# Kernel tuning notes

Hardware: AMD Instinct MI355X
Metric: run time of the kernel (lower is better)

## Reference

```python
import jax, jax.numpy as jnp
import numpy as np

NX, NY, T, TP, D, C = 1024, 1024, 512, 512, 128, 8


def _make_dtw_path(t_len, p_len, rng):
    """Random monotone warping path matrix from (0,0) to (t_len-1,p_len-1), as in init_DTW_matrix."""
    M = np.zeros((t_len, p_len), dtype=np.float32)
    k, l = 0, 0
    M[0, 0] = 1.0
    while (k < t_len - 1) or (l < p_len - 1):
        if k == t_len - 1:
            l += 1
        elif l == p_len - 1:
            k += 1
        else:
            m = rng.integers(3)
            if m == 0:
                k += 1
            elif m == 1:
                l += 1
            else:
                k += 1
                l += 1
        M[k, l] = 1.0
    return M


def setup_inputs() -> dict:
    key = jax.random.key(0)
    kx, ky, kc = jax.random.split(key, 3)
    X = jax.random.normal(kx, (NX, T, D), dtype=jnp.float32)
    Y = jax.random.normal(ky, (NY, TP, D), dtype=jnp.float32)
    classe = jax.random.randint(kc, (NX,), 0, C, dtype=jnp.int32)
    rng = np.random.default_rng(0)
    pi = jnp.asarray(np.stack([_make_dtw_path(T, TP, rng) for _ in range(C)]))  # [C, T, TP]
    return {"X": X, "Y": Y, "pi": pi, "classe": classe}


def reference(X, Y, pi, classe):
    """Fused OT-DTW l2 cost matrix: mat_cost[i,j] = sum_{t,tp,d} pi[cl(i)][t,tp]*(X[i,t,d]-Y[j,tp,d])^2.
    Equivalent to OTDTW.mat_cost_OT with metric='l2' (multi-dim branch), vectorized over classes."""
    pi_i = pi[classe]                              # [NX, T, TP] per-sample path matrix
    row = pi_i.sum(-1)                             # [NX, T]  row sums of path
    col = pi.sum(1)                                # [C, TP]  column sums per class
    C1 = jnp.einsum('itd,it->i', X * X, row)       # [NX]
    C2 = jnp.einsum('jpd,cp->cj', Y * Y, col)      # [C, NY]
    XP = jnp.einsum('itd,itp->ipd', X, pi_i)       # [NX, TP, D]
    C3 = jnp.einsum('ipd,jpd->ij', XP, Y)          # [NX, NY]
    return C1[:, None] + C2[classe] - 2.0 * C3
```

## Files before the change

kernel.cpp:

```cpp
#include <hip/hip_runtime.h>
#include <hip/hip_bf16.h>
#include <stdint.h>

namespace {

constexpr int kNX = 1024, kNY = 1024, kT = 512, kTP = 512, kD = 128, kC = 8;
constexpr int kK = kTP * kD;
constexpr int SPLITK = 16;
constexpr int KCH = kK / SPLITK;
constexpr int BKT = 64;
constexpr int NT = KCH / BKT;

typedef short bf16x8 __attribute__((ext_vector_type(8)));
typedef float f32x4 __attribute__((ext_vector_type(4)));

constexpr size_t OFF_YB  = 0;
constexpr size_t OFF_XP  = OFF_YB + (size_t)kNY * kK * 2;
constexpr size_t OFF_TS  = OFF_XP + (size_t)kNX * kK * 2;
constexpr size_t OFF_TE  = OFF_TS + (size_t)kC * kTP * 4;
constexpr size_t OFF_C1  = OFF_TE + (size_t)kC * kTP * 4;
constexpr size_t OFF_C2  = OFF_C1 + (size_t)kNX * 4;

__device__ __forceinline__ void gload16(const __hip_bfloat16* g, __hip_bfloat16* l) {
    __builtin_amdgcn_global_load_lds(
        (const __attribute__((address_space(1))) unsigned int*)g,
        (__attribute__((address_space(3))) unsigned int*)l, 16, 0, 0);
}

__device__ __forceinline__ unsigned short bf(float x) {
    union { __hip_bfloat16 h; unsigned short u; } cv;
    cv.h = __float2bfloat16(x);
    return cv.u;
}

__global__ void init_ranges(int* __restrict__ ts, int* __restrict__ te,
                            float* __restrict__ C1) {
    const int idx = blockIdx.x * 256 + threadIdx.x;
    if (idx < kC * kTP) { ts[idx] = 0x7fffffff; te[idx] = -1; }
    if (idx < kNX) C1[idx] = 0.f;
}

__global__ void pi_scan(const float* __restrict__ pi, int* __restrict__ ts,
                        int* __restrict__ te) {
    const int c = blockIdx.y;
    const int tbase = blockIdx.x * 64;
    const int p = threadIdx.x;
    const float* pic = pi + (size_t)c * kT * kTP;
    int tmin = 0x7fffffff, tmax = -1;
    for (int tt = 0; tt < 64; ++tt) {
        const int t = tbase + tt;
        float v = pic[(size_t)t * kTP + p];
        if (v != 0.f) { if (t < tmin) tmin = t; tmax = t; }
    }
    if (tmax >= 0) {
        atomicMin(&ts[c * kTP + p], tmin);
        atomicMax(&te[c * kTP + p], tmax);
    }
}

__global__ __launch_bounds__(256) void prep_main(const float* __restrict__ Y,
                                                 const float* __restrict__ X,
                                                 const int* __restrict__ classe,
                                                 const int* __restrict__ ts,
                                                 const int* __restrict__ te,
                                                 __hip_bfloat16* __restrict__ YB,
                                                 __hip_bfloat16* __restrict__ XPB,
                                                 float* __restrict__ C1,
                                                 float* __restrict__ C2) {
    const int bid = blockIdx.x;
    const int tid = threadIdx.x;
    const int sub = tid & 31, g = tid >> 5;

    if (bid < kNY) {
        const int j = bid;
        __shared__ float cntL[kC * kTP];
        for (int idx = tid; idx < kC * kTP; idx += 256)
            cntL[idx] = (float)(te[idx] - ts[idx] + 1);
        __syncthreads();

        const float4* Yj = (const float4*)(Y + (size_t)j * kTP * kD);
        unsigned short* YBj = (unsigned short*)YB + (size_t)j * kTP * kD;
        float c2acc[kC] = {};
        for (int p = g; p < kTP; p += 8) {
            float4 y = Yj[p * 32 + sub];
            ushort4 o;
            o.x = bf(y.x); o.y = bf(y.y); o.z = bf(y.z); o.w = bf(y.w);
            *(ushort4*)(YBj + p * kD + sub * 4) = o;
            float s = y.x * y.x + y.y * y.y + y.z * y.z + y.w * y.w;
            #pragma unroll
            for (int o2 = 16; o2; o2 >>= 1) s += __shfl_xor(s, o2, 32);
            if (sub == 0) {
                #pragma unroll
                for (int c = 0; c < kC; ++c) c2acc[c] += cntL[c * kTP + p] * s;
            }
        }
        __syncthreads();
        __shared__ float c2red[8][kC];
        if (sub == 0) {
            #pragma unroll
            for (int c = 0; c < kC; ++c) c2red[g][c] = c2acc[c];
        }
        __syncthreads();
        if (tid < kC) {
            float s = 0.f;
            #pragma unroll
            for (int q = 0; q < 8; ++q) s += c2red[q][tid];
            C2[tid * kNY + j] = s;
        }
    } else {
        const int b2 = bid - kNY;
        const int x8 = b2 & 7, r = b2 >> 3;
        const int pc = r & 7, i = (r >> 3) * 8 + x8;
        const int c = classe[i];
        const float4* Xi = (const float4*)(X + (size_t)i * kT * kD);
        unsigned short* XPi = (unsigned short*)XPB + (size_t)i * kTP * kD;
        int t0v[8], t1v[8];
        #pragma unroll
        for (int q = 0; q < 8; ++q) {
            const int p = pc * 64 + q * 8 + g;
            t0v[q] = ts[c * kTP + p];
            t1v[q] = te[c * kTP + p];
        }
        float sq = 0.f;
        #pragma unroll
        for (int q = 0; q < 8; ++q) {
            const int p = pc * 64 + q * 8 + g;
            float ax = 0.f, ay = 0.f, az = 0.f, aw = 0.f;
            for (int t = t0v[q]; t <= t1v[q]; ++t) {
                float4 v = Xi[t * 32 + sub];
                ax += v.x; ay += v.y; az += v.z; aw += v.w;
                sq += v.x * v.x + v.y * v.y + v.z * v.z + v.w * v.w;
            }
            ushort4 o;
            o.x = bf(ax); o.y = bf(ay); o.z = bf(az); o.w = bf(aw);
            *(ushort4*)(XPi + p * kD + sub * 4) = o;
        }
        #pragma unroll
        for (int o = 32; o; o >>= 1) sq += __shfl_down(sq, o);
        __shared__ float red[4];
        if ((tid & 63) == 0) red[tid >> 6] = sq;
        __syncthreads();
        if (tid == 0) atomicAdd(&C1[i], red[0] + red[1] + red[2] + red[3]);
    }
}

__global__ void init_out(const float* __restrict__ C1, const float* __restrict__ C2,
                         const int* __restrict__ classe, float* __restrict__ out) {
    const int i = blockIdx.x;
    const float c1 = C1[i];
    const float* c2 = C2 + (size_t)classe[i] * kNY;
    float* o = out + (size_t)i * kNY;
    for (int j = threadIdx.x; j < kNY; j += 256) o[j] = c1 + c2[j];
}

__global__ __launch_bounds__(512, 2) void gemm_c3(const __hip_bfloat16* __restrict__ A,
                                                  const __hip_bfloat16* __restrict__ B,
                                                  float* __restrict__ out) {
    __shared__ __align__(16) char lds[131072];
    __hip_bfloat16* ldsE = (__hip_bfloat16*)lds;

    const int tid = threadIdx.x;
    const int lane = tid & 63, wv = tid >> 6;
    const int wr = wv >> 2, wc = wv & 3;

    const int bid = blockIdx.x;
    const int swz = (bid & 7) * 32 + (bid >> 3);
    const int z = swz >> 4, t16 = swz & 15;
    const int rowBase = (t16 >> 2) * 256;
    const int colBase = (t16 & 3) * 256;
    const size_t k0base = (size_t)z * KCH;

    const int scol = ((tid & 7) * 8) ^ (((tid >> 3) & 7) * 8);
    const __hip_bfloat16* aSrc[4];
    const __hip_bfloat16* bSrc[4];
    int dstE[4];
    #pragma unroll
    for (int q = 0; q < 4; ++q) {
        const int R = q * 64 + (tid >> 3);
        aSrc[q] = A + (size_t)(rowBase + R) * kK + k0base + scol;
        bSrc[q] = B + (size_t)(colBase + R) * kK + k0base + scol;
        dstE[q] = (q * 512 + tid) * 8;
    }

    const int swzR = (lane & 7) << 4;
    const int aLin = (wr * 128 + (lane & 15)) * 128 + ((lane >> 4) << 4);
    const int bLin = (wc * 64 + (lane & 15)) * 128 + ((lane >> 4) << 4);
    const int aB0 = (aLin) ^ swzR, aB1 = (aLin + 64) ^ swzR;
    const int bB0 = (bLin) ^ swzR, bB1 = (bLin + 64) ^ swzR;

    f32x4 acc[8][4] = {};

    #pragma unroll
    for (int q = 0; q < 4; ++q) gload16(aSrc[q], ldsE + dstE[q]);
    #pragma unroll
    for (int q = 0; q < 4; ++q) gload16(bSrc[q], ldsE + 16384 + dstE[q]);

    int buf = 0;
    for (int t = 0; t < NT; ++t) {
        asm volatile("s_waitcnt vmcnt(0)" ::: "memory");
        __builtin_amdgcn_s_barrier();
        asm volatile("" ::: "memory");

        const int koff = (t + 1) * BKT;
        const int bufB = buf * 65536;
        const int nBufE = (buf ^ 1) * 32768;

        if (t + 1 < NT) {
            #pragma unroll
            for (int q = 0; q < 4; ++q) gload16(aSrc[q] + koff, ldsE + nBufE + dstE[q]);
        }

        #pragma unroll
        for (int qd = 0; qd < 4; ++qd) {
            const int mh = qd & 1, nh = qd >> 1;
            bf16x8 af[4][2], bfr[2][2];
            #pragma unroll
            for (int m = 0; m < 4; ++m) {
                af[m][0] = *(const bf16x8*)(lds + bufB + aB0 + mh * 8192 + m * 2048);
                af[m][1] = *(const bf16x8*)(lds + bufB + aB1 + mh * 8192 + m * 2048);
            }
            #pragma unroll
            for (int n = 0; n < 2; ++n) {
                bfr[n][0] = *(const bf16x8*)(lds + bufB + 32768 + bB0 + nh * 4096 + n * 2048);
                bfr[n][1] = *(const bf16x8*)(lds + bufB + 32768 + bB1 + nh * 4096 + n * 2048);
            }
            __builtin_amdgcn_s_setprio(1);
            #pragma unroll
            for (int m = 0; m < 4; ++m)
                #pragma unroll
                for (int n = 0; n < 2; ++n) {
                    acc[mh * 4 + m][nh * 2 + n] = __builtin_amdgcn_mfma_f32_16x16x32_bf16(
                        af[m][0], bfr[n][0], acc[mh * 4 + m][nh * 2 + n], 0, 0, 0);
                    acc[mh * 4 + m][nh * 2 + n] = __builtin_amdgcn_mfma_f32_16x16x32_bf16(
                        af[m][1], bfr[n][1], acc[mh * 4 + m][nh * 2 + n], 0, 0, 0);
                }
            __builtin_amdgcn_s_setprio(0);

            if (qd == 0 && t + 1 < NT) {
                #pragma unroll
                for (int q = 0; q < 4; ++q)
                    gload16(bSrc[q] + koff, ldsE + nBufE + 16384 + dstE[q]);
            }
        }
        buf ^= 1;
    }

    #pragma unroll
    for (int mi = 0; mi < 8; ++mi) {
        #pragma unroll
        for (int ni = 0; ni < 4; ++ni) {
            #pragma unroll
            for (int jj = 0; jj < 4; ++jj) {
                const int R = rowBase + wr * 128 + mi * 16 + (lane >> 4) * 4 + jj;
                const int Cc = colBase + wc * 64 + ni * 16 + (lane & 15);
                atomicAdd(&out[(size_t)R * kNY + Cc], -2.0f * acc[mi][ni][jj]);
            }
        }
    }
}

}

extern "C" void kernel_launch(void* const* d_in, const int* in_sizes, int n_in,
                              void* d_out, int out_size, void* d_ws, size_t ws_size,
                              hipStream_t stream) {
    const float* X = (const float*)d_in[0];
    const float* Y = (const float*)d_in[1];
    const float* pi = (const float*)d_in[2];
    const int* classe = (const int*)d_in[3];
    float* out = (float*)d_out;

    char* ws = (char*)d_ws;
    __hip_bfloat16* YB = (__hip_bfloat16*)(ws + OFF_YB);
    __hip_bfloat16* XPB = (__hip_bfloat16*)(ws + OFF_XP);
    int* ts = (int*)(ws + OFF_TS);
    int* te = (int*)(ws + OFF_TE);
    float* C1 = (float*)(ws + OFF_C1);
    float* C2 = (float*)(ws + OFF_C2);

    init_ranges<<<(kC * kTP + 255) / 256, 256, 0, stream>>>(ts, te, C1);
    pi_scan<<<dim3(kT / 64, kC), kTP, 0, stream>>>(pi, ts, te);
    prep_main<<<kNY + kNX * 8, 256, 0, stream>>>(Y, X, classe, ts, te, YB, XPB, C1, C2);
    init_out<<<kNX, 256, 0, stream>>>(C1, C2, classe, out);
    gemm_c3<<<(kNX / 256) * (kNY / 256) * SPLITK, 512, 0, stream>>>(XPB, YB, out);
}
```

Measured before the change: 339.6 us.

## Use a four-stage LDS ring with BKT=32 in the split-K GEMM; vectorize Y prep

After: 363.0 us. 6.9% more time.

```diff
diff --git a/kernel.cpp b/kernel.cpp
--- a/kernel.cpp
+++ b/kernel.cpp
@@ -8,7 +8,7 @@
 constexpr int kK = kTP * kD;
 constexpr int SPLITK = 16;
 constexpr int KCH = kK / SPLITK;
-constexpr int BKT = 64;
+constexpr int BKT = 32;
 constexpr int NT = KCH / BKT;
 
 typedef short bf16x8 __attribute__((ext_vector_type(8)));
@@ -73,38 +73,40 @@
 
     if (bid < kNY) {
         const int j = bid;
-        __shared__ float cntL[kC * kTP];
-        for (int idx = tid; idx < kC * kTP; idx += 256)
-            cntL[idx] = (float)(te[idx] - ts[idx] + 1);
+        __shared__ float cntL[kTP * kC];
+        for (int idx = tid; idx < kC * kTP; idx += 256) {
+            const int c = idx >> 9, p = idx & 511;
+            cntL[p * 8 + c] = (float)(te[idx] - ts[idx] + 1);
+        }
         __syncthreads();
 
-        const float4* Yj = (const float4*)(Y + (size_t)j * kTP * kD);
+        const int si = sub & 15, half = sub >> 4;
+        const float* Yj = Y + (size_t)j * kTP * kD;
         unsigned short* YBj = (unsigned short*)YB + (size_t)j * kTP * kD;
-        float c2acc[kC] = {};
-        for (int p = g; p < kTP; p += 8) {
-            float4 y = Yj[p * 32 + sub];
-            ushort4 o;
-            o.x = bf(y.x); o.y = bf(y.y); o.z = bf(y.z); o.w = bf(y.w);
-            *(ushort4*)(YBj + p * kD + sub * 4) = o;
-            float s = y.x * y.x + y.y * y.y + y.z * y.z + y.w * y.w;
-            #pragma unroll
-            for (int o2 = 16; o2; o2 >>= 1) s += __shfl_xor(s, o2, 32);
-            if (sub == 0) {
-                #pragma unroll
-                for (int c = 0; c < kC; ++c) c2acc[c] += cntL[c * kTP + p] * s;
-            }
-        }
+        float c2acc = 0.f;
+        for (int pb = g * 2; pb < kTP; pb += 16) {
+            const int p = pb + half;
+            const float4* src = (const float4*)(Yj + (size_t)p * kD + si * 8);
+            float4 v0 = src[0], v1 = src[1];
+            union { ushort4 h[2]; uint4 q; } o;
+            o.h[0].x = bf(v0.x); o.h[0].y = bf(v0.y); o.h[0].z = bf(v0.z); o.h[0].w = bf(v0.w);
+            o.h[1].x = bf(v1.x); o.h[1].y = bf(v1.y); o.h[1].z = bf(v1.z); o.h[1].w = bf(v1.w);
+            *(uint4*)(YBj + (size_t)p * kD + si * 8) = o.q;
+            float s = v0.x * v0.x + v0.y * v0.y + v0.z * v0.z + v0.w * v0.w
+                    + v1.x * v1.x + v1.y * v1.y + v1.z * v1.z + v1.w * v1.w;
+            s += __shfl_xor(s, 1, 32);
+            s += __shfl_xor(s, 2, 32);
+            s += __shfl_xor(s, 4, 32);
+            s += __shfl_xor(s, 8, 32);
+            if (si < 8) c2acc += cntL[p * 8 + si] * s;
+        }
+        __shared__ float c2red[16][8];
+        if (si < 8) c2red[g * 2 + half][si] = c2acc;
         __syncthreads();
-        __shared__ float c2red[8][kC];
-        if (sub == 0) {
-            #pragma unroll
-            for (int c = 0; c < kC; ++c) c2red[g][c] = c2acc[c];
-        }
-        __syncthreads();
-        if (tid < kC) {
+        if (tid < 8) {
             float s = 0.f;
             #pragma unroll
-            for (int q = 0; q < 8; ++q) s += c2red[q][tid];
+            for (int q = 0; q < 16; ++q) s += c2red[q][tid];
             C2[tid * kNY + j] = s;
         }
     } else {
@@ -170,80 +172,65 @@
     const int colBase = (t16 & 3) * 256;
     const size_t k0base = (size_t)z * KCH;
 
-    const int scol = ((tid & 7) * 8) ^ (((tid >> 3) & 7) * 8);
-    const __hip_bfloat16* aSrc[4];
-    const __hip_bfloat16* bSrc[4];
-    int dstE[4];
-    #pragma unroll
-    for (int q = 0; q < 4; ++q) {
-        const int R = q * 64 + (tid >> 3);
-        aSrc[q] = A + (size_t)(rowBase + R) * kK + k0base + scol;
-        bSrc[q] = B + (size_t)(colBase + R) * kK + k0base + scol;
-        dstE[q] = (q * 512 + tid) * 8;
-    }
-
-    const int swzR = (lane & 7) << 4;
-    const int aLin = (wr * 128 + (lane & 15)) * 128 + ((lane >> 4) << 4);
-    const int bLin = (wc * 64 + (lane & 15)) * 128 + ((lane >> 4) << 4);
-    const int aB0 = (aLin) ^ swzR, aB1 = (aLin + 64) ^ swzR;
-    const int bB0 = (bLin) ^ swzR, bB1 = (bLin + 64) ^ swzR;
+    const int sk = ((tid & 3) ^ ((tid >> 3) & 3)) * 8;
+    const int rA0 = tid >> 2, rA1 = 128 + (tid >> 2);
+    const __hip_bfloat16* aSrc0 = A + (size_t)(rowBase + rA0) * kK + k0base + sk;
+    const __hip_bfloat16* aSrc1 = A + (size_t)(rowBase + rA1) * kK + k0base + sk;
+    const __hip_bfloat16* bSrc0 = B + (size_t)(colBase + rA0) * kK + k0base + sk;
+    const __hip_bfloat16* bSrc1 = B + (size_t)(colBase + rA1) * kK + k0base + sk;
+    const int dst0 = tid * 8, dst1 = 4096 + tid * 8;
+
+#define STAGE(s) do {                                                          \
+    const int _ko = (s) * BKT;                                                 \
+    __hip_bfloat16* _b = ldsE + ((s) & 3) * 16384;                             \
+    gload16(aSrc0 + _ko, _b + dst0);                                           \
+    gload16(aSrc1 + _ko, _b + dst1);                                           \
+    gload16(bSrc0 + _ko, _b + 8192 + dst0);                                    \
+    gload16(bSrc1 + _ko, _b + 8192 + dst1);                                    \
+} while (0)
+
+    const int rl = lane & 15;
+    const int kphys = (((lane >> 4) ^ ((rl >> 1) & 3)) << 4);
+    const int aByte = (wr * 128 + rl) * 64 + kphys;
+    const int bByte = 16384 + (wc * 64 + rl) * 64 + kphys;
 
     f32x4 acc[8][4] = {};
 
-    #pragma unroll
-    for (int q = 0; q < 4; ++q) gload16(aSrc[q], ldsE + dstE[q]);
-    #pragma unroll
-    for (int q = 0; q < 4; ++q) gload16(bSrc[q], ldsE + 16384 + dstE[q]);
-
-    int buf = 0;
-    for (int t = 0; t < NT; ++t) {
-        asm volatile("s_waitcnt vmcnt(0)" ::: "memory");
+#define COMPUTE(t) do {                                                        \
+    const char* _bb = lds + ((t) & 3) * 32768;                                 \
+    bf16x8 _bfr[4];                                                            \
+    _Pragma("unroll")                                                          \
+    for (int n = 0; n < 4; ++n)                                                \
+        _bfr[n] = *(const bf16x8*)(_bb + bByte + n * 1024);                    \
+    __builtin_amdgcn_s_setprio(1);                                             \
+    _Pragma("unroll")                                                          \
+    for (int m = 0; m < 8; ++m) {                                              \
+        bf16x8 _af = *(const bf16x8*)(_bb + aByte + m * 1024);                 \
+        _Pragma("unroll")                                                      \
+        for (int n = 0; n < 4; ++n)                                            \
+            acc[m][n] = __builtin_amdgcn_mfma_f32_16x16x32_bf16(               \
+                _af, _bfr[n], acc[m][n], 0, 0, 0);                             \
+    }                                                                          \
+    __builtin_amdgcn_s_setprio(0);                                             \
+} while (0)
+
+    STAGE(0); STAGE(1); STAGE(2);
+
+    for (int t = 0; t < NT - 2; ++t) {
+        asm volatile("s_waitcnt vmcnt(8)" ::: "memory");
         __builtin_amdgcn_s_barrier();
-        asm volatile("" ::: "memory");
-
-        const int koff = (t + 1) * BKT;
-        const int bufB = buf * 65536;
-        const int nBufE = (buf ^ 1) * 32768;
-
-        if (t + 1 < NT) {
-            #pragma unroll
-            for (int q = 0; q < 4; ++q) gload16(aSrc[q] + koff, ldsE + nBufE + dstE[q]);
-        }
-
-        #pragma unroll
-        for (int qd = 0; qd < 4; ++qd) {
-            const int mh = qd & 1, nh = qd >> 1;
-            bf16x8 af[4][2], bfr[2][2];
-            #pragma unroll
-            for (int m = 0; m < 4; ++m) {
-                af[m][0] = *(const bf16x8*)(lds + bufB + aB0 + mh * 8192 + m * 2048);
-                af[m][1] = *(const bf16x8*)(lds + bufB + aB1 + mh * 8192 + m * 2048);
-            }
-            #pragma unroll
-            for (int n = 0; n < 2; ++n) {
-                bfr[n][0] = *(const bf16x8*)(lds + bufB + 32768 + bB0 + nh * 4096 + n * 2048);
-                bfr[n][1] = *(const bf16x8*)(lds + bufB + 32768 + bB1 + nh * 4096 + n * 2048);
-            }
-            __builtin_amdgcn_s_setprio(1);
-            #pragma unroll
-            for (int m = 0; m < 4; ++m)
-                #pragma unroll
-                for (int n = 0; n < 2; ++n) {
-                    acc[mh * 4 + m][nh * 2 + n] = __builtin_amdgcn_mfma_f32_16x16x32_bf16(
-                        af[m][0], bfr[n][0], acc[mh * 4 + m][nh * 2 + n], 0, 0, 0);
-                    acc[mh * 4 + m][nh * 2 + n] = __builtin_amdgcn_mfma_f32_16x16x32_bf16(
-                        af[m][1], bfr[n][1], acc[mh * 4 + m][nh * 2 + n], 0, 0, 0);
-                }
-            __builtin_amdgcn_s_setprio(0);
-
-            if (qd == 0 && t + 1 < NT) {
-                #pragma unroll
-                for (int q = 0; q < 4; ++q)
-                    gload16(bSrc[q] + koff, ldsE + nBufE + 16384 + dstE[q]);
-            }
-        }
-        buf ^= 1;
-    }
+        if (t + 3 < NT) STAGE(t + 3);
+        COMPUTE(t);
+    }
+    asm volatile("s_waitcnt vmcnt(4)" ::: "memory");
+    __builtin_amdgcn_s_barrier();
+    COMPUTE(NT - 2);
+    asm volatile("s_waitcnt vmcnt(0)" ::: "memory");
+    __builtin_amdgcn_s_barrier();
+    COMPUTE(NT - 1);
+
+#undef STAGE
+#undef COMPUTE
 
     #pragma unroll
     for (int mi = 0; mi < 8; ++mi) {
```
